# Kernel optimization log

Measured on AMD Instinct MI355X. Metric: run time of the kernel, lower is better.

## Reference

```python
import jax, jax.numpy as jnp
import numpy as np

B, N, D = 8, 2048, 1024

def setup_inputs() -> dict:
    key = jax.random.key(0)
    ks = jax.random.split(key, 7)
    s = 1.0 / np.sqrt(D)
    return {
        "x": jax.random.normal(ks[0], (B, N, D), dtype=jnp.float32),
        "Wq": jax.random.uniform(ks[1], (D, D), jnp.float32, -s, s),
        "bq": jax.random.uniform(ks[2], (D,), jnp.float32, -s, s),
        "Wk": jax.random.uniform(ks[3], (D, D), jnp.float32, -s, s),
        "bk": jax.random.uniform(ks[4], (D,), jnp.float32, -s, s),
        "Wv": jax.random.uniform(ks[5], (D, D), jnp.float32, -s, s),
        "bv": jax.random.uniform(ks[6], (D,), jnp.float32, -s, s),
    }

def reference(x, Wq, bq, Wk, bk, Wv, bv):
    # torch nn.Linear: y = x @ W.T + b
    q = jnp.einsum('bnd,ed->bne', x, Wq) + bq
    k = jnp.einsum('bnd,ed->bne', x, Wk) + bk
    v = jnp.einsum('bnd,ed->bne', x, Wv) + bv
    # NOTE: original applies NO 1/sqrt(d) scaling
    scores = jnp.einsum('bnd,bmd->bnm', q, k)  # [B, N, N]
    probs = jax.nn.softmax(scores, axis=-1)
    return jnp.einsum('bnm,bmd->bnd', probs, v)
```

## Files before the change

### kernel.cpp

```cpp
#include <hip/hip_runtime.h>


typedef _Float16 f16;
typedef _Float16 f16x4 __attribute__((ext_vector_type(4)));
typedef _Float16 f16x8 __attribute__((ext_vector_type(8)));
typedef float f32x4 __attribute__((ext_vector_type(4)));

#define Nn_ 2048
#define Dd 1024

typedef const __attribute__((address_space(1))) void gvoid;
typedef __attribute__((address_space(3))) void lvoid;

__device__ __forceinline__ void glds16(const void* g, void* l) {
    __builtin_amdgcn_global_load_lds((gvoid*)g, (lvoid*)l, 16, 0, 0);
}

__global__ void cvt_kernel(const float4* __restrict__ in, f16x4* __restrict__ out, int n4) {
    int i = blockIdx.x * 256 + threadIdx.x;
    if (i >= n4) return;
    float4 f = in[i];
    f16x4 h;
    h.x = (_Float16)f.x; h.y = (_Float16)f.y; h.z = (_Float16)f.z; h.w = (_Float16)f.w;
    out[i] = h;
}

__global__ void concat_bias(const float* __restrict__ bq, const float* __restrict__ bk,
                            const float* __restrict__ bv, float* __restrict__ o) {
    int i = blockIdx.x * 256 + threadIdx.x;
    if (i >= 3072) return;
    o[i] = (i < 1024) ? bq[i] : (i < 2048 ? bk[i - 1024] : bv[i - 2048]);
}

__global__ __launch_bounds__(256) void gemm_bt(
    const f16* __restrict__ A, const f16* __restrict__ Bm,
    const float* __restrict__ bias, void* __restrict__ Cout,
    f16* __restrict__ qh, f16* __restrict__ kh, f16* __restrict__ vT,
    int K, int lda, int ldb, int ldc, int mode,
    long aStride, long bStride, long cStride)
{
    __shared__ f16 sm[16384];
    const int tid = threadIdx.x;
    const int lane = tid & 63, wid = tid >> 6;
    const int quad = lane >> 4, l16 = lane & 15;
    const int wm = (wid >> 1) * 64, wn = (wid & 1) * 64;
    const long m0 = (long)blockIdx.x * 128, n0 = (long)blockIdx.y * 128;
    const int bz = blockIdx.z;
    A += (long)bz * aStride;
    Bm += (long)bz * bStride;

    const int ca = tid, cb = tid + 256;
    const long ar0 = m0 + (ca >> 2), ar1 = m0 + (cb >> 2);
    const long br0 = n0 + (ca >> 2), br1 = n0 + (cb >> 2);
    const int col0 = (ca & 3) * 8, col1 = (cb & 3) * 8;

    const f16* pa0 = A + ar0 * lda + col0;
    const f16* pa1 = A + ar1 * lda + col1;
    const f16* pb0 = Bm + br0 * ldb + col0;
    const f16* pb1 = Bm + br1 * ldb + col1;

    f32x4 acc[4][4];
#pragma unroll
    for (int i = 0; i < 4; i++)
#pragma unroll
        for (int j = 0; j < 4; j++) acc[i][j] = 0.0f;

    glds16(pa0, sm + ca * 8);
    glds16(pa1, sm + cb * 8);
    glds16(pb0, sm + 4096 + ca * 8);
    glds16(pb1, sm + 4096 + cb * 8);

    int cur = 0;
    for (int k0 = 0; k0 < K; k0 += 32) {
        __syncthreads();
        if (k0 + 32 < K) {
            f16* dst = sm + ((cur ^ 1) << 13);
            glds16(pa0 + k0 + 32, dst + ca * 8);
            glds16(pa1 + k0 + 32, dst + cb * 8);
            glds16(pb0 + k0 + 32, dst + 4096 + ca * 8);
            glds16(pb1 + k0 + 32, dst + 4096 + cb * 8);
        }
        const f16* As = sm + (cur << 13);
        const f16* Bs = As + 4096;
        f16x8 af[4], bf[4];
#pragma unroll
        for (int rt = 0; rt < 4; rt++)
            af[rt] = *(const f16x8*)(As + (wm + rt * 16 + l16) * 32 + quad * 8);
#pragma unroll
        for (int ct = 0; ct < 4; ct++)
            bf[ct] = *(const f16x8*)(Bs + (wn + ct * 16 + l16) * 32 + quad * 8);
#pragma unroll
        for (int rt = 0; rt < 4; rt++)
#pragma unroll
            for (int ct = 0; ct < 4; ct++)
                acc[rt][ct] = __builtin_amdgcn_mfma_f32_16x16x32_f16(af[rt], bf[ct], acc[rt][ct], 0, 0, 0);
        cur ^= 1;
    }

    if (mode == 2) {
        float* O = (float*)Cout + (long)bz * cStride;
#pragma unroll
        for (int ct = 0; ct < 4; ct++) {
            long n = n0 + wn + ct * 16 + l16;
#pragma unroll
            for (int rt = 0; rt < 4; rt++) {
                long mb = m0 + wm + rt * 16 + quad * 4;
#pragma unroll
                for (int r = 0; r < 4; r++)
                    O[(mb + r) * ldc + n] = acc[rt][ct][r];
            }
        }
    } else {
        if (blockIdx.y < 16) {
            f16* O = (blockIdx.y < 8) ? qh : kh;
#pragma unroll
            for (int ct = 0; ct < 4; ct++) {
                long n = n0 + wn + ct * 16 + l16;
                float bs = bias[n];
                long n1 = n & 1023;
#pragma unroll
                for (int rt = 0; rt < 4; rt++) {
                    long mb = m0 + wm + rt * 16 + quad * 4;
#pragma unroll
                    for (int r = 0; r < 4; r++)
                        O[(mb + r) * 1024 + n1] = (f16)(acc[rt][ct][r] + bs);
                }
            }
        } else {
            const long nb = n0 - 2048;
            const long vbase = (m0 >> 11) * (long)(Dd * Nn_) + (m0 & 2047);
#pragma unroll
            for (int h = 0; h < 2; ++h) {
                __syncthreads();
                if ((wid & 1) == h) {
#pragma unroll
                    for (int ct = 0; ct < 4; ++ct) {
                        int cl = ct * 16 + l16;
                        float bs = bias[n0 + h * 64 + cl];
#pragma unroll
                        for (int rt = 0; rt < 4; rt++) {
                            int row = wm + rt * 16 + quad * 4;
#pragma unroll
                            for (int r = 0; r < 4; r++)
                                sm[cl * 136 + row + r] = (f16)(acc[rt][ct][r] + bs);
                        }
                    }
                }
                __syncthreads();
                const int rowi = tid >> 2, c4 = (tid & 3) * 32;
                f16* dst = vT + vbase + (nb + h * 64 + rowi) * (long)Nn_ + c4;
                const f16* src = sm + rowi * 136 + c4;
#pragma unroll
                for (int j = 0; j < 4; ++j)
                    *(f16x8*)(dst + j * 8) = *(const f16x8*)(src + j * 8);
            }
        }
    }
}

__global__ __launch_bounds__(256) void softmax_rows(float* __restrict__ S) {
    const int row = blockIdx.x * 4 + (threadIdx.x >> 6);
    const int lane = threadIdx.x & 63;
    float* Sr = S + (long)row * 2048;
    const float4* R4 = (const float4*)Sr;
    float4 t[8];
#pragma unroll
    for (int i = 0; i < 8; i++) t[i] = R4[lane + 64 * i];
    float mx = -1e30f;
#pragma unroll
    for (int i = 0; i < 8; i++)
        mx = fmaxf(mx, fmaxf(fmaxf(t[i].x, t[i].y), fmaxf(t[i].z, t[i].w)));
#pragma unroll
    for (int off = 1; off < 64; off <<= 1) mx = fmaxf(mx, __shfl_xor(mx, off, 64));
    float se = 0.0f;
#pragma unroll
    for (int i = 0; i < 8; i++) {
        t[i].x = __expf(t[i].x - mx); t[i].y = __expf(t[i].y - mx);
        t[i].z = __expf(t[i].z - mx); t[i].w = __expf(t[i].w - mx);
        se += t[i].x + t[i].y + t[i].z + t[i].w;
    }
#pragma unroll
    for (int off = 1; off < 64; off <<= 1) se += __shfl_xor(se, off, 64);
    const float li = 1.0f / se;
    f16x4* P4 = (f16x4*)Sr;
#pragma unroll
    for (int i = 0; i < 8; i++) {
        f16x4 h;
        h.x = (_Float16)(t[i].x * li); h.y = (_Float16)(t[i].y * li);
        h.z = (_Float16)(t[i].z * li); h.w = (_Float16)(t[i].w * li);
        P4[lane + 64 * i] = h;
    }
}

extern "C" void kernel_launch(void* const* d_in, const int* in_sizes, int n_in,
                              void* d_out, int out_size, void* d_ws, size_t ws_size,
                              hipStream_t stream) {
    const float* x  = (const float*)d_in[0];
    const float* Wq = (const float*)d_in[1];
    const float* bq = (const float*)d_in[2];
    const float* Wk = (const float*)d_in[3];
    const float* bk = (const float*)d_in[4];
    const float* Wv = (const float*)d_in[5];
    const float* bv = (const float*)d_in[6];

    f16* wsh = (f16*)d_ws;
    dim3 blk(256);
    const bool full = ws_size >= 234881024ULL;

    if (full) {
        f16* qh  = wsh;
        f16* kh  = wsh + 16777216;
        f16* vT  = wsh + 33554432;
        float* S = (float*)(wsh + 50331648);
        f16* xh  = wsh + 50331648;
        f16* Wh  = wsh + 67108864;
        float* bqkv = (float*)(wsh + 70254592);

        cvt_kernel<<<16384, 256, 0, stream>>>((const float4*)x, (f16x4*)xh, 4194304);
        cvt_kernel<<<1024, 256, 0, stream>>>((const float4*)Wq, (f16x4*)Wh, 262144);
        cvt_kernel<<<1024, 256, 0, stream>>>((const float4*)Wk, (f16x4*)(Wh + 1048576), 262144);
        cvt_kernel<<<1024, 256, 0, stream>>>((const float4*)Wv, (f16x4*)(Wh + 2097152), 262144);
        concat_bias<<<12, 256, 0, stream>>>(bq, bk, bv, bqkv);

        gemm_bt<<<dim3(128, 24, 1), blk, 0, stream>>>(
            xh, Wh, bqkv, nullptr, qh, kh, vT,
            1024, 1024, 1024, 0, 3, 0, 0, 0);
        gemm_bt<<<dim3(16, 16, 8), blk, 0, stream>>>(
            qh, kh, nullptr, S, nullptr, nullptr, nullptr,
            1024, 1024, 1024, 2048, 2,
            (long)Nn_ * Dd, (long)Nn_ * Dd, (long)Nn_ * Nn_);
        softmax_rows<<<4096, 256, 0, stream>>>(S);
        gemm_bt<<<dim3(16, 8, 8), blk, 0, stream>>>(
            (const f16*)S, vT, nullptr, d_out, nullptr, nullptr, nullptr,
            2048, 4096, 2048, 1024, 2,
            (long)Nn_ * 4096, (long)Dd * Nn_, (long)Nn_ * Dd);
    } else {
        f16* xh  = wsh;
        f16* Wh  = wsh + 16777216;
        float* bqkv = (float*)(wsh + 19922944);
        f16* qh  = wsh + 19929088;
        f16* kh  = qh + 16777216;
        f16* vT  = kh + 16777216;
        float* S = (float*)(vT + 16777216);

        cvt_kernel<<<16384, 256, 0, stream>>>((const float4*)x, (f16x4*)xh, 4194304);
        cvt_kernel<<<1024, 256, 0, stream>>>((const float4*)Wq, (f16x4*)Wh, 262144);
        cvt_kernel<<<1024, 256, 0, stream>>>((const float4*)Wk, (f16x4*)(Wh + 1048576), 262144);
        cvt_kernel<<<1024, 256, 0, stream>>>((const float4*)Wv, (f16x4*)(Wh + 2097152), 262144);
        concat_bias<<<12, 256, 0, stream>>>(bq, bk, bv, bqkv);

        gemm_bt<<<dim3(128, 24, 1), blk, 0, stream>>>(
            xh, Wh, bqkv, nullptr, qh, kh, vT,
            1024, 1024, 1024, 0, 3, 0, 0, 0);

        for (int h = 0; h < 2; ++h) {
            const long b0 = 4L * h;
            gemm_bt<<<dim3(16, 16, 4), blk, 0, stream>>>(
                qh + b0 * Nn_ * Dd, kh + b0 * Nn_ * Dd, nullptr, S,
                nullptr, nullptr, nullptr,
                1024, 1024, 1024, 2048, 2,
                (long)Nn_ * Dd, (long)Nn_ * Dd, (long)Nn_ * Nn_);
            softmax_rows<<<2048, 256, 0, stream>>>(S);
            gemm_bt<<<dim3(16, 8, 4), blk, 0, stream>>>(
                (const f16*)S, vT + b0 * Dd * Nn_, nullptr,
                (float*)d_out + b0 * Nn_ * Dd, nullptr, nullptr, nullptr,
                2048, 4096, 2048, 1024, 2,
                (long)Nn_ * 4096, (long)Dd * Nn_, (long)Nn_ * Dd);
        }
    }
}
```

Baseline: 490.4 us.

## Triple-buffer GEMM LDS loads with vmcnt waits and XOR-swizzle shared layout

Moves the GEMM main loop from double to triple buffering. Two k-tiles stay in flight, and the barrier is an explicit s_waitcnt vmcnt(4) plus s_barrier, so the kernel waits only for the oldest tile. It also XOR-swizzles the 16-byte column chunks in LDS, on both the global_load_lds destinations and the fragment reads, to reduce bank conflicts. LDS use grows from 32 KB to 48 KB per block, which may lower occupancy. The hand-written waitcnt depends on the count of outstanding loads being correct.

```diff
diff --git a/kernel.cpp b/kernel.cpp
--- a/kernel.cpp
+++ b/kernel.cpp
@@ -14,6 +14,12 @@
 
 __device__ __forceinline__ void glds16(const void* g, void* l) {
     __builtin_amdgcn_global_load_lds((gvoid*)g, (lvoid*)l, 16, 0, 0);
+}
+__device__ __forceinline__ void bar_vm4() {
+    asm volatile("s_waitcnt vmcnt(4)\n\ts_barrier" ::: "memory");
+}
+__device__ __forceinline__ void bar_vm0() {
+    asm volatile("s_waitcnt vmcnt(0)\n\ts_barrier" ::: "memory");
 }
 
 __global__ void cvt_kernel(const float4* __restrict__ in, f16x4* __restrict__ out, int n4) {
@@ -39,7 +45,7 @@
     int K, int lda, int ldb, int ldc, int mode,
     long aStride, long bStride, long cStride)
 {
-    __shared__ f16 sm[16384];
+    __shared__ f16 sm[24576];
     const int tid = threadIdx.x;
     const int lane = tid & 63, wid = tid >> 6;
     const int quad = lane >> 4, l16 = lane & 15;
@@ -52,49 +58,60 @@
     const int ca = tid, cb = tid + 256;
     const long ar0 = m0 + (ca >> 2), ar1 = m0 + (cb >> 2);
     const long br0 = n0 + (ca >> 2), br1 = n0 + (cb >> 2);
-    const int col0 = (ca & 3) * 8, col1 = (cb & 3) * 8;
+    const int col0 = ((ca & 3) ^ ((ca >> 3) & 3)) * 8;
+    const int col1 = ((cb & 3) ^ ((cb >> 3) & 3)) * 8;
 
     const f16* pa0 = A + ar0 * lda + col0;
     const f16* pa1 = A + ar1 * lda + col1;
     const f16* pb0 = Bm + br0 * ldb + col0;
     const f16* pb1 = Bm + br1 * ldb + col1;
 
+    const int fo = (quad ^ ((l16 >> 1) & 3)) * 8;
+
     f32x4 acc[4][4];
 #pragma unroll
     for (int i = 0; i < 4; i++)
 #pragma unroll
         for (int j = 0; j < 4; j++) acc[i][j] = 0.0f;
 
+    const int nk = K >> 5;
     glds16(pa0, sm + ca * 8);
     glds16(pa1, sm + cb * 8);
     glds16(pb0, sm + 4096 + ca * 8);
     glds16(pb1, sm + 4096 + cb * 8);
+    if (nk > 1) {
+        glds16(pa0 + 32, sm + 8192 + ca * 8);
+        glds16(pa1 + 32, sm + 8192 + cb * 8);
+        glds16(pb0 + 32, sm + 12288 + ca * 8);
+        glds16(pb1 + 32, sm + 12288 + cb * 8);
+    }
 
     int cur = 0;
-    for (int k0 = 0; k0 < K; k0 += 32) {
-        __syncthreads();
-        if (k0 + 32 < K) {
-            f16* dst = sm + ((cur ^ 1) << 13);
-            glds16(pa0 + k0 + 32, dst + ca * 8);
-            glds16(pa1 + k0 + 32, dst + cb * 8);
-            glds16(pb0 + k0 + 32, dst + 4096 + ca * 8);
-            glds16(pb1 + k0 + 32, dst + 4096 + cb * 8);
-        }
-        const f16* As = sm + (cur << 13);
+    for (int it = 0; it < nk; ++it) {
+        if (it + 1 < nk) bar_vm4(); else bar_vm0();
+        if (it + 2 < nk) {
+            f16* dst = sm + ((cur >= 1) ? (cur - 1) : (cur + 2)) * 8192;
+            const int ko = (it + 2) * 32;
+            glds16(pa0 + ko, dst + ca * 8);
+            glds16(pa1 + ko, dst + cb * 8);
+            glds16(pb0 + ko, dst + 4096 + ca * 8);
+            glds16(pb1 + ko, dst + 4096 + cb * 8);
+        }
+        const f16* As = sm + cur * 8192;
         const f16* Bs = As + 4096;
         f16x8 af[4], bf[4];
 #pragma unroll
         for (int rt = 0; rt < 4; rt++)
-            af[rt] = *(const f16x8*)(As + (wm + rt * 16 + l16) * 32 + quad * 8);
+            af[rt] = *(const f16x8*)(As + (wm + rt * 16 + l16) * 32 + fo);
 #pragma unroll
         for (int ct = 0; ct < 4; ct++)
-            bf[ct] = *(const f16x8*)(Bs + (wn + ct * 16 + l16) * 32 + quad * 8);
+            bf[ct] = *(const f16x8*)(Bs + (wn + ct * 16 + l16) * 32 + fo);
 #pragma unroll
         for (int rt = 0; rt < 4; rt++)
 #pragma unroll
             for (int ct = 0; ct < 4; ct++)
                 acc[rt][ct] = __builtin_amdgcn_mfma_f32_16x16x32_f16(af[rt], bf[ct], acc[rt][ct], 0, 0, 0);
-        cur ^= 1;
+        cur = (cur == 2) ? 0 : cur + 1;
     }
 
     if (mode == 2) {
```

Result: faster. 460.6 us (-6.1%).
